# Performance work log

Measured on AMD Instinct MI355X. Metric: run time of the kernel, lower is better.

Reference implementation:

```python
import jax, jax.numpy as jnp
import numpy as np

B, DIM, HEADS, HEAD_DIM = 4, 768, 8, 96
THW = (8, 28, 28)
N_TOK = THW[0] * THW[1] * THW[2] + 1  # +1 cls token = 6273
HIDDEN = 4 * DIM
STRIDE = (1, 2, 2)
SCALE = HEAD_DIM ** -0.5


def layernorm(x, w, b, eps=1e-5):
    mu = x.mean(-1, keepdims=True)
    var = ((x - mu) ** 2).mean(-1, keepdims=True)
    return (x - mu) / jnp.sqrt(var + eps) * w + b


def conv_pool(x, w):
    # depthwise 3D conv: x [BN, C, T, H, W], w [C, 1, 3, 3, 3], stride (1,2,2), pad 1
    return jax.lax.conv_general_dilated(
        x, w, window_strides=STRIDE, padding=[(1, 1), (1, 1), (1, 1)],
        dimension_numbers=('NCDHW', 'OIDHW', 'NCDHW'),
        feature_group_count=x.shape[1])


def attn_pool(x, conv_w, norm_w, norm_b):
    # x: [B, h, N, d]; pool spatial tokens (excluding cls), then LayerNorm(head_dim)
    cls, xs = x[:, :, :1], x[:, :, 1:]
    b, h, _, d = xs.shape
    t, hh, ww = THW
    xs = xs.reshape(b * h, t, hh, ww, d).transpose(0, 4, 1, 2, 3)  # [bh, d, t, h, w]
    xs = conv_pool(xs, conv_w)
    l_pooled = xs.shape[2] * xs.shape[3] * xs.shape[4]
    xs = xs.reshape(b, h, d, l_pooled).transpose(0, 1, 3, 2)  # [B, h, L, d]
    xs = jnp.concatenate([cls, xs], axis=2)
    return layernorm(xs, norm_w, norm_b)


def max_pool_skip(x):
    # residual-path MaxPool3d: kernel (1,3,3), stride (1,2,2), pad (0,1,1); cls excluded
    cls, xs = x[:, :1], x[:, 1:]
    b, _, c = xs.shape
    t, hh, ww = THW
    xs = xs.reshape(b, t, hh, ww, c)
    xs = jax.lax.reduce_window(
        xs, -jnp.inf, jax.lax.max,
        (1, 1, 3, 3, 1), (1, 1, 2, 2, 1),
        [(0, 0), (0, 0), (1, 1), (1, 1), (0, 0)])
    xs = xs.reshape(b, -1, c)
    return jnp.concatenate([cls, xs], axis=1)


def setup_inputs() -> dict:
    key = jax.random.key(0)
    ks = jax.random.split(key, 16)
    s = 0.02
    inp = {
        'x': jax.random.normal(ks[0], (B, N_TOK, DIM), jnp.float32),
        'n1_w': jnp.ones((DIM,), jnp.float32), 'n1_b': jnp.zeros((DIM,), jnp.float32),
        'wq': jax.random.normal(ks[1], (DIM, DIM), jnp.float32) * s,
        'bq': jnp.zeros((DIM,), jnp.float32),
        'wk': jax.random.normal(ks[2], (DIM, DIM), jnp.float32) * s,
        'bk': jnp.zeros((DIM,), jnp.float32),
        'wv': jax.random.normal(ks[3], (DIM, DIM), jnp.float32) * s,
        'bv': jnp.zeros((DIM,), jnp.float32),
        'pq_w': jax.random.normal(ks[4], (HEAD_DIM, 1, 3, 3, 3), jnp.float32) * s,
        'pk_w': jax.random.normal(ks[5], (HEAD_DIM, 1, 3, 3, 3), jnp.float32) * s,
        'pv_w': jax.random.normal(ks[6], (HEAD_DIM, 1, 3, 3, 3), jnp.float32) * s,
        'nq_w': jnp.ones((HEAD_DIM,), jnp.float32), 'nq_b': jnp.zeros((HEAD_DIM,), jnp.float32),
        'nk_w': jnp.ones((HEAD_DIM,), jnp.float32), 'nk_b': jnp.zeros((HEAD_DIM,), jnp.float32),
        'nv_w': jnp.ones((HEAD_DIM,), jnp.float32), 'nv_b': jnp.zeros((HEAD_DIM,), jnp.float32),
        'proj_w': jax.random.normal(ks[7], (DIM, DIM), jnp.float32) * s,
        'proj_b': jnp.zeros((DIM,), jnp.float32),
        'n2_w': jnp.ones((DIM,), jnp.float32), 'n2_b': jnp.zeros((DIM,), jnp.float32),
        'fc1_w': jax.random.normal(ks[8], (HIDDEN, DIM), jnp.float32) * s,
        'fc1_b': jnp.zeros((HIDDEN,), jnp.float32),
        'fc2_w': jax.random.normal(ks[9], (DIM, HIDDEN), jnp.float32) * s,
        'fc2_b': jnp.zeros((DIM,), jnp.float32),
    }
    return inp


def reference(x, n1_w, n1_b, wq, bq, wk, bk, wv, bv, pq_w, pk_w, pv_w,
              nq_w, nq_b, nk_w, nk_b, nv_w, nv_b, proj_w, proj_b,
              n2_w, n2_b, fc1_w, fc1_b, fc2_w, fc2_b):
    b, n, _ = x.shape
    xn = layernorm(x, n1_w, n1_b)
    # q/k/v projections -> [B, h, N, d]
    q = (xn @ wq.T + bq).reshape(b, n, HEADS, HEAD_DIM).transpose(0, 2, 1, 3)
    k = (xn @ wk.T + bk).reshape(b, n, HEADS, HEAD_DIM).transpose(0, 2, 1, 3)
    v = (xn @ wv.T + bv).reshape(b, n, HEADS, HEAD_DIM).transpose(0, 2, 1, 3)
    q = attn_pool(q, pq_w, nq_w, nq_b)
    k = attn_pool(k, pk_w, nk_w, nk_b)
    v = attn_pool(v, pv_w, nv_w, nv_b)
    attn = jax.nn.softmax(jnp.einsum('bhqd,bhkd->bhqk', q, k) * SCALE, axis=-1)
    o = jnp.einsum('bhqk,bhkd->bhqd', attn, v)
    nq = o.shape[2]
    o = o.transpose(0, 2, 1, 3).reshape(b, nq, DIM)
    o = o @ proj_w.T + proj_b
    # residual with pooled skip
    x2 = max_pool_skip(x) + o
    xn2 = layernorm(x2, n2_w, n2_b)
    m = jax.nn.gelu(xn2 @ fc1_w.T + fc1_b, approximate=False) @ fc2_w.T + fc2_b
    return x2 + m
```

## Files before the change

kernel.cpp:

```cpp
#include <hip/hip_runtime.h>
#include <math.h>

#define B_ 4
#define NTOK 6273
#define DIMD 768
#define HEADS 8
#define HD 96
#define NPOOL 1569
#define NPAD 1600
#define HID 3072
#define MROWS (B_*NTOK)
#define M2 (B_*NPOOL)
#define SCALE_ 0.10206207261596575f

typedef float f32x4 __attribute__((ext_vector_type(4)));
typedef short s16x8 __attribute__((ext_vector_type(8)));
typedef short s16x4 __attribute__((ext_vector_type(4)));
typedef unsigned u32x3 __attribute__((ext_vector_type(3)));

__device__ __forceinline__ short f2bf(float f){
  unsigned u = __builtin_bit_cast(unsigned, f);
  u = (u + 0x7fffu + ((u >> 16) & 1u)) >> 16;
  return (short)u;
}
__device__ __forceinline__ float bf2f(short s){
  unsigned u = ((unsigned)(unsigned short)s) << 16;
  return __builtin_bit_cast(float, u);
}
__device__ __forceinline__ float bfsel(unsigned u, int hi){
  unsigned r = hi ? (u & 0xffff0000u) : (u << 16);
  return __builtin_bit_cast(float, r);
}
__device__ __forceinline__ unsigned pack2(float lo, float hi){
  return (unsigned)(unsigned short)f2bf(lo) | ((unsigned)(unsigned short)f2bf(hi) << 16);
}

__device__ __forceinline__ void gld16(const void* g, void* l){
  __builtin_amdgcn_global_load_lds((const __attribute__((address_space(1))) unsigned*)g,
                                   (__attribute__((address_space(3))) unsigned*)l, 16, 0, 0);
}

#if defined(__has_builtin)
#if __has_builtin(__builtin_amdgcn_mfma_f32_16x16x16bf16_1k)
#define MFMA16K(a,b,c) __builtin_amdgcn_mfma_f32_16x16x16bf16_1k(a,b,c,0,0,0)
#endif
#endif
#ifndef MFMA16K
__device__ __forceinline__ f32x4 mfma16k_asm(s16x4 a, s16x4 b, f32x4 c){
  asm volatile("v_mfma_f32_16x16x16_bf16 %0, %1, %2, %0\n\ts_nop 7\n\ts_nop 7"
               : "+v"(c) : "v"(a), "v"(b));
  return c;
}
#define MFMA16K(a,b,c) mfma16k_asm(a,b,c)
#endif

template<int NT>
__device__ __forceinline__ float block_sum(float v, float* red){
  int t = threadIdx.x;
  red[t] = v; __syncthreads();
  #pragma unroll
  for (int s = NT/2; s > 0; s >>= 1){
    if (t < s) red[t] += red[t+s];
    __syncthreads();
  }
  float r = red[0];
  __syncthreads();
  return r;
}

__device__ __forceinline__ unsigned xcd_serial(unsigned bid, unsigned nwg){
  unsigned q = nwg >> 3, r8 = nwg & 7;
  unsigned xcd = bid & 7, idx = bid >> 3;
  return (xcd < r8 ? xcd*(q+1) : r8*(q+1) + (xcd-r8)*q) + idx;
}

template<int STR, int STC>
__device__ __forceinline__ void tile_decode(unsigned serial, int& rowT, int& colT){
  const int nStC = (int)gridDim.x / STC;
  int st = (int)serial / (STR*STC);
  int t  = (int)serial - st*(STR*STC);
  int stR = st / nStC, stC = st - stR*nStC;
  int c = t / STR, r = t - c*STR;
  rowT = stR*STR + r;
  colT = stC*STC + c;
}

__global__ void castw(const float* s0,const float* s1,const float* s2,const float* s3,
                      const float* s4,const float* s5,
                      short* d0,short* d1,short* d2,short* d3,short* d4,short* d5){
  const float* s; short* d; int n;
  switch(blockIdx.y){
    case 0: s=s0; d=d0; n=589824; break;
    case 1: s=s1; d=d1; n=589824; break;
    case 2: s=s2; d=d2; n=589824; break;
    case 3: s=s3; d=d3; n=589824; break;
    case 4: s=s4; d=d4; n=2359296; break;
    default: s=s5; d=d5; n=2359296; break;
  }
  for (int i = blockIdx.x*blockDim.x + threadIdx.x; i < n; i += gridDim.x*blockDim.x)
    d[i] = f2bf(s[i]);
}

__global__ __launch_bounds__(256) void packb(const float* b0, const float* b1, const float* b2, float* o){
  int i = blockIdx.x*256 + threadIdx.x;
  if (i < 768) o[i] = b0[i];
  else if (i < 1536) o[i] = b1[i-768];
  else if (i < 2304) o[i] = b2[i-1536];
}

__global__ __launch_bounds__(256) void ln768(const float* __restrict__ x, const float* __restrict__ w,
                      const float* __restrict__ b, short* __restrict__ out){
  int row = blockIdx.x*4 + (threadIdx.x >> 6);
  int lane = threadIdx.x & 63;
  const float* xr = x + (size_t)row*DIMD + lane*12;
  f32x4 v0 = *(const f32x4*)(xr);
  f32x4 v1 = *(const f32x4*)(xr + 4);
  f32x4 v2 = *(const f32x4*)(xr + 8);
  float v[12] = { v0[0],v0[1],v0[2],v0[3], v1[0],v1[1],v1[2],v1[3], v2[0],v2[1],v2[2],v2[3] };
  float s = 0.f;
  #pragma unroll
  for (int j=0;j<12;j++) s += v[j];
  #pragma unroll
  for (int m=1; m<64; m<<=1) s += __shfl_xor(s, m);
  float mu = s * (1.f/768.f);
  float sq = 0.f;
  #pragma unroll
  for (int j=0;j<12;j++){ float d = v[j]-mu; sq += d*d; }
  #pragma unroll
  for (int m=1; m<64; m<<=1) sq += __shfl_xor(sq, m);
  float rstd = rsqrtf(sq*(1.f/768.f) + 1e-5f);
  int c0 = lane*12;
  float o[12];
  #pragma unroll
  for (int j=0;j<12;j++) o[j] = (v[j]-mu)*rstd*w[c0+j] + b[c0+j];
  unsigned* po = (unsigned*)(out + (size_t)row*DIMD + c0);
  #pragma unroll
  for (int k=0;k<6;k++) po[k] = pack2(o[2*k], o[2*k+1]);
}

__global__ __launch_bounds__(512) void gemm8(const short* __restrict__ A, const short* __restrict__ Bw,
                        const float* __restrict__ bias, short* __restrict__ Cb,
                        int M, int N, int K){
  __shared__ short lds[4][16384];
  int tid = threadIdx.x;
  int w = tid >> 6, lane = tid & 63;
  int l15 = lane & 15, g = (lane >> 4) & 3;
  int wr = w >> 2, wc = w & 3;

  unsigned nwg = gridDim.x * gridDim.y;
  unsigned bid = blockIdx.y * gridDim.x + blockIdx.x;
  unsigned serial = bid;
  if (nwg >= 512) serial = xcd_serial(bid, nwg);
  int rowBase = (int)(serial / gridDim.x) * 256;
  int colBase = (int)(serial % gridDim.x) * 256;

  const short* pa[2]; const short* pb[2];
  #pragma unroll
  for (int j=0;j<2;j++){
    int mr = rowBase + (w + j*8)*16 + l15; if (mr >= M) mr = M-1;
    int nr = colBase + (w + j*8)*16 + l15;
    pa[j] = A  + (size_t)mr*K + g*8;
    pb[j] = Bw + (size_t)nr*K + g*8;
  }
  int sd = tid*8;

  auto stage = [&](int slot, int p){
    int koff = p*32;
    short* base = &lds[slot][0];
    #pragma unroll
    for (int j=0;j<2;j++){
      gld16(pa[j] + koff, base + sd + j*4096);
      gld16(pb[j] + koff, base + 8192 + sd + j*4096);
    }
  };

  f32x4 acc[8][4] = {};
  int np = K >> 5;
  stage(0, 0);
  if (np > 1) stage(1, 1);
  if (np > 2) stage(2, 2);
  for (int p = 0; p < np; p++){
    if (p <= np-3)
      asm volatile("s_waitcnt vmcnt(8)" ::: "memory");
    else if (p == np-2)
      asm volatile("s_waitcnt vmcnt(4)" ::: "memory");
    else
      asm volatile("s_waitcnt vmcnt(0)" ::: "memory");
    __builtin_amdgcn_s_barrier();
    if (p + 3 < np) stage((p+3)&3, p+3);
    const short* lA = &lds[p&3][0];
    const short* lB = lA + 8192;
    s16x8 bfr[4];
    #pragma unroll
    for (int nf=0; nf<4; nf++)
      bfr[nf] = *(const s16x8*)(lB + (wc*4+nf)*512 + lane*8);
    __builtin_amdgcn_s_setprio(1);
    #pragma unroll
    for (int mf=0; mf<8; mf++){
      s16x8 af = *(const s16x8*)(lA + (wr*8+mf)*512 + lane*8);
      #pragma unroll
      for (int nf=0; nf<4; nf++)
        acc[mf][nf] = __builtin_amdgcn_mfma_f32_16x16x32_bf16(af, bfr[nf], acc[mf][nf], 0,0,0);
    }
    __builtin_amdgcn_s_setprio(0);
  }

  __syncthreads();
  short* ldsC = &lds[0][0];
  #pragma unroll
  for (int mf=0; mf<8; mf++){
    int rowL0 = wr*128 + mf*16 + g*4;
    #pragma unroll
    for (int nf=0; nf<4; nf++){
      int colL = wc*64 + nf*16 + l15;
      float bv = bias[colBase + colL];
      int ch = colL >> 3, in8 = colL & 7;
      #pragma unroll
      for (int r=0;r<4;r++){
        int rL = rowL0 + r;
        int chs = ch ^ ((rL >> 2) & 7);
        ldsC[rL*256 + chs*8 + in8] = f2bf(acc[mf][nf][r] + bv);
      }
    }
  }
  __syncthreads();
  int ch2 = tid & 31, rg = tid >> 5;
  #pragma unroll
  for (int i=0;i<16;i++){
    int rowL = rg + i*16;
    int chs = ch2 ^ ((rowL >> 2) & 7);
    s16x8 v = *(const s16x8*)(ldsC + rowL*256 + chs*8);
    int rr = rowBase + rowL;
    if (rr < M) *(s16x8*)(Cb + (size_t)rr*N + colBase + ch2*8) = v;
  }
}

template<int GELU, int OUTBF16, int RESID, int STR, int STC>
__global__ __launch_bounds__(256) void gemm_bt(const short* __restrict__ A, const short* __restrict__ Bw,
                        const float* __restrict__ bias, const float* __restrict__ resid,
                        float* __restrict__ Cf, short* __restrict__ Cb,
                        int M, int N, int K){
  __shared__ short lds[3][8192];
  int tid = threadIdx.x;
  int lane = tid & 63, wv = tid >> 6;
  int wr = wv >> 1, wc = wv & 1;
  int l15 = lane & 15, g = lane >> 4;

  unsigned nwg = gridDim.x * gridDim.y;
  unsigned bid = blockIdx.y * gridDim.x + blockIdx.x;
  unsigned serial = xcd_serial(bid, nwg);
  int rowT, colT;
  tile_decode<STR,STC>(serial, rowT, colT);
  int rowBase = rowT * 128;
  int colBase = colT * 128;

  f32x4 acc[4][4] = {};
  int srow = (tid & 15) | ((tid >> 6) << 4);
  int scol = ((tid >> 4) & 3) * 8;
  int ldsoff = tid * 8;

  int ar0 = rowBase + srow;      if (ar0 >= M) ar0 = M-1;
  int ar1 = rowBase + srow + 64; if (ar1 >= M) ar1 = M-1;
  int br0 = colBase + srow;
  const short* pa0 = A  + (size_t)ar0*K + scol;
  const short* pa1 = A  + (size_t)ar1*K + scol;
  const short* pb0 = Bw + (size_t)br0*K + scol;
  const short* pb1 = Bw + (size_t)(br0+64)*K + scol;

  auto stage = [&](int s, int kt){
    gld16(pa0 + kt, &lds[s][ldsoff]);
    gld16(pa1 + kt, &lds[s][ldsoff + 2048]);
    gld16(pb0 + kt, &lds[s][4096 + ldsoff]);
    gld16(pb1 + kt, &lds[s][4096 + ldsoff + 2048]);
  };

  int nk = K >> 5;
  stage(0, 0);
  if (nk > 1) stage(1, 32);
  for (int kt = 0; kt < nk; kt++){
    int cur = kt % 3;
    if (kt + 2 < nk){
      stage((kt+2)%3, (kt+2)*32);
      asm volatile("s_waitcnt vmcnt(8)" ::: "memory");
    } else if (kt + 1 < nk){
      asm volatile("s_waitcnt vmcnt(4)" ::: "memory");
    } else {
      asm volatile("s_waitcnt vmcnt(0)" ::: "memory");
    }
    __builtin_amdgcn_s_barrier();
    const short* la = lds[cur];
    const short* lb = lds[cur] + 4096;
    s16x8 af[4], bfr[4];
    #pragma unroll
    for (int m=0;m<4;m++) af[m]  = *(const s16x8*)(la + (wr*4 + m)*512 + g*128 + l15*8);
    #pragma unroll
    for (int n=0;n<4;n++) bfr[n] = *(const s16x8*)(lb + (wc*4 + n)*512 + g*128 + l15*8);
    #pragma unroll
    for (int m=0;m<4;m++)
      #pragma unroll
      for (int n=0;n<4;n++)
        acc[m][n] = __builtin_amdgcn_mfma_f32_16x16x32_bf16(af[m], bfr[n], acc[m][n], 0,0,0);
    __builtin_amdgcn_s_barrier();
  }

  if (OUTBF16){
    short* ldsC = &lds[0][0];
    #pragma unroll
    for (int n=0;n<4;n++){
      int colL = wc*64 + n*16 + l15;
      float bv = bias[colBase + colL];
      #pragma unroll
      for (int m=0;m<4;m++){
        #pragma unroll
        for (int r=0;r<4;r++){
          int rowL = wr*64 + m*16 + g*4 + r;
          float v = acc[m][n][r] + bv;
          if (GELU) v = 0.5f*v*(1.f + erff(v*0.70710678118654752f));
          int ch = colL >> 3, in8 = colL & 7;
          int chs = ch ^ (((rowL >> 2) & 3) << 2);
          ldsC[rowL*128 + chs*8 + in8] = f2bf(v);
        }
      }
    }
    __syncthreads();
    int ch = tid & 15, rg = tid >> 4;
    #pragma unroll
    for (int i=0;i<8;i++){
      int rowL = rg + i*16;
      int chs = ch ^ (((rowL >> 2) & 3) << 2);
      s16x8 v = *(const s16x8*)(ldsC + rowL*128 + chs*8);
      int rr = rowBase + rowL;
      if (rr < M) *(s16x8*)(Cb + (size_t)rr*N + colBase + ch*8) = v;
    }
  } else {
    #pragma unroll
    for (int m=0;m<4;m++){
      int row = rowBase + wr*64 + m*16 + g*4;
      #pragma unroll
      for (int n=0;n<4;n++){
        int col = colBase + wc*64 + n*16 + l15;
        float bv = bias[col];
        #pragma unroll
        for (int r=0;r<4;r++){
          int rr = row + r;
          if (rr < M){
            float v = acc[m][n][r] + bv;
            if (GELU) v = 0.5f*v*(1.f + erff(v*0.70710678118654752f));
            if (RESID) v += resid[(size_t)rr*N + col];
            Cf[(size_t)rr*N + col] = v;
          }
        }
      }
    }
  }
}

__global__ __launch_bounds__(256, 2) void pool_conv3(
    const short* __restrict__ raw,
    const float* __restrict__ cwq, const float* __restrict__ cwk, const float* __restrict__ cwv,
    const float* __restrict__ nqw, const float* __restrict__ nqb,
    const float* __restrict__ nkw, const float* __restrict__ nkb,
    const float* __restrict__ nvw, const float* __restrict__ nvb,
    short* __restrict__ qo, short* __restrict__ ko, short* __restrict__ vo){
  unsigned nwg = gridDim.x * gridDim.y * gridDim.z;
  unsigned lin = (blockIdx.z*gridDim.y + blockIdx.y)*gridDim.x + blockIdx.x;
  unsigned serial = xcd_serial(lin, nwg);
  int ho = (int)(serial % 14);
  unsigned rest = serial / 14;
  int bh = (int)(rest & 31);
  int z  = (int)(rest >> 5);
  int t = threadIdx.x;
  int g = t >> 4;
  if (g >= 14) return;
  int s = t & 15, d = s*6;
  const float* cw = (z==0) ? cwq : (z==1) ? cwk : cwv;
  const float* nw = (z==0) ? nqw : (z==1) ? nkw : nvw;
  const float* nb = (z==0) ? nqb : (z==1) ? nkb : nvb;
  const short* base = raw + (size_t)(bh>>3)*NTOK*2304 + z*768 + (bh&7)*96 + d;
  float acc[8][6] = {};
  #pragma unroll
  for (int dh=0; dh<3; dh++){
    int ih = 2*ho - 1 + dh;
    if (ih < 0 || ih >= 28) continue;
    #pragma unroll
    for (int dw=0; dw<3; dw++){
      int iw = 2*g - 1 + dw;
      if (iw < 0 || iw >= 28) continue;
      float w[3][6];
      #pragma unroll
      for (int dt=0; dt<3; dt++)
        #pragma unroll
        for (int j=0;j<6;j++)
          w[dt][j] = cw[(d+j)*27 + dt*9 + dh*3 + dw];
      #pragma unroll
      for (int it=0; it<8; it++){
        u32x3 u = *(const u32x3*)(base + (size_t)(1 + (it*28+ih)*28 + iw)*2304);
        float in[6] = { bfsel(u[0],0), bfsel(u[0],1), bfsel(u[1],0),
                        bfsel(u[1],1), bfsel(u[2],0), bfsel(u[2],1) };
        #pragma unroll
        for (int dt=0; dt<3; dt++){
          int to = it + 1 - dt;
          if (to < 0 || to > 7) continue;
          #pragma unroll
          for (int j=0;j<6;j++) acc[to][j] = fmaf(in[j], w[dt][j], acc[to][j]);
        }
      }
    }
  }
  float nwv[6], nbv[6];
  #pragma unroll
  for (int j=0;j<6;j++){ nwv[j] = nw[d+j]; nbv[j] = nb[d+j]; }
  #pragma unroll
  for (int to=0; to<8; to++){
    float sm = acc[to][0]+acc[to][1]+acc[to][2]+acc[to][3]+acc[to][4]+acc[to][5];
    #pragma unroll
    for (int m=1; m<16; m<<=1) sm += __shfl_xor(sm, m);
    float mu = sm*(1.f/96.f);
    float vr = 0.f;
    #pragma unroll
    for (int j=0;j<6;j++){ float dd = acc[to][j]-mu; vr += dd*dd; }
    #pragma unroll
    for (int m=1; m<16; m<<=1) vr += __shfl_xor(vr, m);
    float rstd = rsqrtf(vr*(1.f/96.f) + 1e-5f);
    int tok = 1 + to*196 + ho*14 + g;
    if (z == 0){
      short o[6];
      #pragma unroll
      for (int j=0;j<6;j++) o[j] = f2bf((acc[to][j]-mu)*rstd*nwv[j] + nbv[j]);
      unsigned* q32 = (unsigned*)(qo + ((size_t)bh*NPAD + tok)*96 + d);
      #pragma unroll
      for (int w2=0; w2<3; w2++)
        q32[w2] = (unsigned)(unsigned short)o[2*w2] | ((unsigned)(unsigned short)o[2*w2+1] << 16);
    } else if (z == 1){
      size_t kb = (size_t)bh*NPAD*96 + (size_t)(tok>>4)*1536 + (tok&15)*8;
      #pragma unroll
      for (int j=0;j<6;j++){
        int dj = d + j;
        ko[kb + (dj>>5)*512 + ((dj>>3)&3)*128 + (dj&7)] = f2bf((acc[to][j]-mu)*rstd*nwv[j] + nbv[j]);
      }
    } else {
      size_t vb = (size_t)bh*NPAD*96 + (size_t)(tok>>6)*6144 + ((tok>>4)&3)*256 + ((tok>>2)&3)*64 + (tok&3);
      #pragma unroll
      for (int j=0;j<6;j++){
        int dj = d + j;
        vo[vb + (dj>>4)*1024 + (dj&15)*4] = f2bf((acc[to][j]-mu)*rstd*nwv[j] + nbv[j]);
      }
    }
  }
}

__global__ __launch_bounds__(128) void cls3(
    const short* __restrict__ raw,
    const float* __restrict__ nqw, const float* __restrict__ nqb,
    const float* __restrict__ nkw, const float* __restrict__ nkb,
    const float* __restrict__ nvw, const float* __restrict__ nvb,
    short* __restrict__ qo, short* __restrict__ ko, short* __restrict__ vo){
  int b = blockIdx.x, t = threadIdx.x;
  int h = t >> 4, s = t & 15, d = s*6;
  int bh = b*8 + h;
  const float* nws[3] = { nqw, nkw, nvw };
  const float* nbs[3] = { nqb, nkb, nvb };
  #pragma unroll
  for (int ten=0; ten<3; ten++){
    const short* row = raw + (size_t)b*NTOK*2304 + ten*768 + h*96 + d;
    u32x3 u = *(const u32x3*)(row);
    float a[6] = { bfsel(u[0],0), bfsel(u[0],1), bfsel(u[1],0), bfsel(u[1],1), bfsel(u[2],0), bfsel(u[2],1) };
    float sm = a[0]+a[1]+a[2]+a[3]+a[4]+a[5];
    #pragma unroll
    for (int m=1; m<16; m<<=1) sm += __shfl_xor(sm, m);
    float mu = sm*(1.f/96.f);
    float vr2 = 0.f;
    #pragma unroll
    for (int j=0;j<6;j++){ float dd = a[j]-mu; vr2 += dd*dd; }
    #pragma unroll
    for (int m=1; m<16; m<<=1) vr2 += __shfl_xor(vr2, m);
    float rstd = rsqrtf(vr2*(1.f/96.f) + 1e-5f);
    #pragma unroll
    for (int j=0;j<6;j++){
      int dj = d + j;
      short o = f2bf((a[j]-mu)*rstd*nws[ten][dj] + nbs[ten][dj]);
      if (ten == 0)      qo[((size_t)bh*NPAD)*96 + dj] = o;
      else if (ten == 1) ko[(size_t)bh*NPAD*96 + (dj>>5)*512 + ((dj>>3)&3)*128 + (dj&7)] = o;
      else               vo[(size_t)bh*NPAD*96 + (dj>>4)*1024 + (dj&15)*4] = o;
    }
  }
}

__global__ __launch_bounds__(96) void padfill(short* __restrict__ qo, short* __restrict__ ko, short* __restrict__ vo){
  int tok = NPOOL + blockIdx.x;
  int bh = blockIdx.y;
  int d = threadIdx.x;
  qo[((size_t)bh*NPAD + tok)*96 + d] = 0;
  size_t kb = (size_t)bh*NPAD*96 + (size_t)(tok>>4)*1536 + (tok&15)*8;
  ko[kb + (d>>5)*512 + ((d>>3)&3)*128 + (d&7)] = 0;
  size_t vb = (size_t)bh*NPAD*96 + (size_t)(tok>>6)*6144 + ((tok>>4)&3)*256 + ((tok>>2)&3)*64 + (tok&3);
  vo[vb + (d>>4)*1024 + (d&15)*4] = 0;
}

__global__ __launch_bounds__(512) void attn_k(const short* __restrict__ qp, const short* __restrict__ kp,
                       const short* __restrict__ vp, short* __restrict__ oattn){
  const float M0 = 6.0f;
  __shared__ short lkv[2][12288];
  unsigned nwg = gridDim.x * gridDim.y;
  unsigned bid0 = blockIdx.y * gridDim.x + blockIdx.x;
  unsigned serial = xcd_serial(bid0, nwg);
  int bh = (int)(serial / 13);
  int qblk = (int)(serial - (unsigned)bh*13);
  int b = bh >> 3, h = bh & 7;
  int tid = threadIdx.x;
  int lane = tid & 63, wv = tid >> 6;
  int l15 = lane & 15, g = lane >> 4;
  int qi = qblk*128 + wv*16 + l15;
  int qi_ld = qi < NPAD ? qi : NPAD-1;
  const short* qbase = qp + (size_t)bh*NPAD*HD;
  const short* kbase = kp + (size_t)bh*NPAD*HD;
  const short* vbase = vp + (size_t)bh*NPAD*HD;
  s16x8 qf[3];
  #pragma unroll
  for (int f=0; f<3; f++)
    qf[f] = *(const s16x8*)(qbase + (size_t)qi_ld*HD + f*32 + g*8);

  auto stage = [&](int bsel, int t){
    #pragma unroll
    for (int i=0;i<3;i++){
      int off = i*4096 + tid*8;
      const short* src = (off < 6144) ? (kbase + t*6144 + off) : (vbase + t*6144 + off - 6144);
      gld16(src, &lkv[bsel][off]);
    }
  };

  f32x4 accO[6] = {};
  float tsum = 0.f;

  stage(0, 0);
  asm volatile("s_waitcnt vmcnt(0)" ::: "memory");
  __builtin_amdgcn_s_barrier();

  for (int kt = 0; kt < 25; kt++){
    int cur = kt & 1;
    if (kt < 24){
      stage(cur^1, kt+1);
      asm volatile("s_waitcnt vmcnt(3)" ::: "memory");
    } else {
      asm volatile("s_waitcnt vmcnt(0)" ::: "memory");
    }
    __builtin_amdgcn_s_barrier();

    const short* lkc = &lkv[cur][0];
    const short* lvc = &lkv[cur][6144];
    f32x4 sacc[4];
    #pragma unroll
    for (int sub=0; sub<4; sub++){
      sacc[sub] = (f32x4){0.f,0.f,0.f,0.f};
      #pragma unroll
      for (int f=0; f<3; f++){
        s16x8 kf = *(const s16x8*)(lkc + sub*1536 + f*512 + lane*8);
        sacc[sub] = __builtin_amdgcn_mfma_f32_16x16x32_bf16(kf, qf[f], sacc[sub], 0,0,0);
      }
    }
    s16x4 pf[4];
    if (kt < 24){
      #pragma unroll
      for (int sub=0; sub<4; sub++){
        #pragma unroll
        for (int r=0; r<4; r++){
          float p = __expf(sacc[sub][r]*SCALE_ - M0);
          tsum += p;
          pf[sub][r] = f2bf(p);
        }
      }
    } else {
      #pragma unroll
      for (int sub=0; sub<4; sub++){
        #pragma unroll
        for (int r=0; r<4; r++){
          int ki = kt*64 + sub*16 + g*4 + r;
          float p = (ki < NPOOL) ? __expf(sacc[sub][r]*SCALE_ - M0) : 0.f;
          tsum += p;
          pf[sub][r] = f2bf(p);
        }
      }
    }
    #pragma unroll
    for (int dt=0; dt<6; dt++){
      #pragma unroll
      for (int sub=0; sub<4; sub++){
        s16x4 vf = *(const s16x4*)(lvc + dt*1024 + sub*256 + lane*4);
        accO[dt] = MFMA16K(vf, pf[sub], accO[dt]);
      }
    }
    __builtin_amdgcn_s_barrier();
  }

  tsum += __shfl_xor(tsum, 16);
  tsum += __shfl_xor(tsum, 32);
  if (qi < NPOOL){
    float inv = 1.f / tsum;
    #pragma unroll
    for (int dt=0; dt<6; dt++){
      #pragma unroll
      for (int r=0; r<4; r++){
        int dd = dt*16 + g*4 + r;
        oattn[((size_t)b*NPOOL + qi)*DIMD + h*96 + dd] = f2bf(accO[dt][r] * inv);
      }
    }
  }
}

__global__ __launch_bounds__(256) void skip_ln2(const float* __restrict__ x, const float* __restrict__ oproj,
                         const float* __restrict__ w, const float* __restrict__ bb,
                         float* __restrict__ x2, short* __restrict__ xn2){
  unsigned nwg = gridDim.x * gridDim.y;
  unsigned bid = blockIdx.y * gridDim.x + blockIdx.x;
  unsigned serial = xcd_serial(bid, nwg);
  int b = (int)(serial / NPOOL);
  int tok = (int)(serial - (unsigned)b*NPOOL);
  int t = threadIdx.x;
  __shared__ float red[256];
  float v[3];
  int ot = tok - 1;
  int to = ot/196, rem = ot%196, ho = rem/14, wo = rem%14;
  #pragma unroll
  for (int i=0;i<3;i++){
    int c = t + i*256;
    float mv;
    if (tok == 0){
      mv = x[(size_t)b*NTOK*DIMD + c];
    } else {
      mv = -INFINITY;
      #pragma unroll
      for (int dh=0; dh<3; dh++){
        int ih = 2*ho - 1 + dh; if (ih < 0 || ih >= 28) continue;
        #pragma unroll
        for (int dw=0; dw<3; dw++){
          int iw = 2*wo - 1 + dw; if (iw < 0 || iw >= 28) continue;
          int n = 1 + (to*28 + ih)*28 + iw;
          mv = fmaxf(mv, x[((size_t)b*NTOK + n)*DIMD + c]);
        }
      }
    }
    float val = mv + oproj[((size_t)b*NPOOL + tok)*DIMD + c];
    x2[((size_t)b*NPOOL + tok)*DIMD + c] = val;
    v[i] = val;
  }
  float s = v[0]+v[1]+v[2];
  s = block_sum<256>(s, red);
  float mu = s * (1.f/768.f);
  float sq = 0.f;
  #pragma unroll
  for (int i=0;i<3;i++){ float d = v[i]-mu; sq += d*d; }
  sq = block_sum<256>(sq, red);
  float rstd = rsqrtf(sq*(1.f/768.f) + 1e-5f);
  #pragma unroll
  for (int i=0;i<3;i++){
    int c = t + i*256;
    xn2[((size_t)b*NPOOL + tok)*DIMD + c] = f2bf((v[i]-mu)*rstd*w[c] + bb[c]);
  }
}

extern "C" void kernel_launch(void* const* d_in, const int* in_sizes, int n_in,
                              void* d_out, int out_size, void* d_ws, size_t ws_size,
                              hipStream_t stream){
  (void)in_sizes; (void)n_in; (void)out_size; (void)ws_size;
  const float* x      = (const float*)d_in[0];
  const float* n1_w   = (const float*)d_in[1];
  const float* n1_b   = (const float*)d_in[2];
  const float* wq     = (const float*)d_in[3];
  const float* bq     = (const float*)d_in[4];
  const float* wk     = (const float*)d_in[5];
  const float* bk     = (const float*)d_in[6];
  const float* wv     = (const float*)d_in[7];
  const float* bv     = (const float*)d_in[8];
  const float* pq_w   = (const float*)d_in[9];
  const float* pk_w   = (const float*)d_in[10];
  const float* pv_w   = (const float*)d_in[11];
  const float* nq_w   = (const float*)d_in[12];
  const float* nq_b   = (const float*)d_in[13];
  const float* nk_w   = (const float*)d_in[14];
  const float* nk_b   = (const float*)d_in[15];
  const float* nv_w   = (const float*)d_in[16];
  const float* nv_b   = (const float*)d_in[17];
  const float* proj_w = (const float*)d_in[18];
  const float* proj_b = (const float*)d_in[19];
  const float* n2_w   = (const float*)d_in[20];
  const float* n2_b   = (const float*)d_in[21];
  const float* fc1_w  = (const float*)d_in[22];
  const float* fc1_b  = (const float*)d_in[23];
  const float* fc2_w  = (const float*)d_in[24];
  const float* fc2_b  = (const float*)d_in[25];
  float* out = (float*)d_out;

  char* ws = (char*)d_ws;
  size_t off = 0;
  auto take = [&](size_t bytes)->char*{
    char* p = ws + off; off = (off + bytes + 255) & ~(size_t)255; return p;
  };
  short* xn  = (short*)take(38541312);
  short* wqb = (short*)take(1179648);
  short* wkb = (short*)take(1179648);
  short* wvb = (short*)take(1179648);
  short* wpb = (short*)take(1179648);
  short* w1b = (short*)take(4718592);
  short* w2b = (short*)take(4718592);
  float* bcat= (float*)take(9216);
  char*  big = take(115623936);
  short* qkv  = (short*)(big);
  short* oattn= (short*)(big);
  float* oproj= (float*)(big + 9639936);
  float* x2   = (float*)(big + 28919808);
  short* xn2  = (short*)(big + 48199680);
  short* h1   = (short*)(big + 57839616);
  short* qp   = (short*)take(9830400);
  short* kp   = (short*)take(9830400);
  short* vT   = (short*)take(9830400);

  castw<<<dim3(2304,6), 256, 0, stream>>>(wq,wk,wv,proj_w,fc1_w,fc2_w, wqb,wkb,wvb,wpb,w1b,w2b);
  packb<<<9, 256, 0, stream>>>(bq, bk, bv, bcat);
  ln768<<<6273, 256, 0, stream>>>(x, n1_w, n1_b, xn);

  gemm8<<<dim3(9,99), 512, 0, stream>>>(xn, wqb, bcat, qkv, MROWS, 2304, 768);

  pool_conv3<<<dim3(32,14,3), 256, 0, stream>>>(qkv, pq_w, pk_w, pv_w,
                                                nq_w, nq_b, nk_w, nk_b, nv_w, nv_b, qp, kp, vT);
  cls3<<<dim3(B_), 128, 0, stream>>>(qkv, nq_w, nq_b, nk_w, nk_b, nv_w, nv_b, qp, kp, vT);
  padfill<<<dim3(31,32), 96, 0, stream>>>(qp, kp, vT);

  attn_k<<<dim3(13,32), 512, 0, stream>>>(qp, kp, vT, oattn);

  gemm_bt<0,0,0,10,6><<<dim3(6,50), 256, 0, stream>>>(oattn, wpb, proj_b, nullptr, oproj, nullptr, M2, 768, 768);

  skip_ln2<<<dim3(NPOOL,B_), 256, 0, stream>>>(x, oproj, n2_w, n2_b, x2, xn2);

  gemm_bt<1,1,0,10,8><<<dim3(24,50), 256, 0, stream>>>(xn2, w1b, fc1_b, nullptr, nullptr, h1, M2, HID, 768);
  gemm_bt<0,0,1,2,3><<<dim3(6,50), 256, 0, stream>>>(h1, w2b, fc2_b, x2, out, nullptr, M2, 768, HID);
}
```

Baseline: 614.6 us.

## Restructure gemm8 main loop into an 8-phase ping-pong schedule with 64-wide K tiles

```diff
diff --git a/kernel.cpp b/kernel.cpp
--- a/kernel.cpp
+++ b/kernel.cpp
@@ -138,14 +138,45 @@
   for (int k=0;k<6;k++) po[k] = pack2(o[2*k], o[2*k+1]);
 }
 
+template<int MH>
+__device__ __forceinline__ void ld_af(s16x8 (&af)[4][2], const short* lA, int lane){
+  #pragma unroll
+  for (int m2=0;m2<4;m2++)
+    #pragma unroll
+    for (int ks=0;ks<2;ks++)
+      af[m2][ks] = *(const s16x8*)(lA + ((MH*4+m2)*2+ks)*512 + lane*8);
+}
+template<int NH>
+__device__ __forceinline__ void ld_bf(s16x8 (&bf)[2][2], const short* lB, int wc1, int lane){
+  #pragma unroll
+  for (int n2=0;n2<2;n2++)
+    #pragma unroll
+    for (int ks=0;ks<2;ks++)
+      bf[n2][ks] = *(const s16x8*)(lB + ((wc1*4+NH*2+n2)*2+ks)*512 + lane*8);
+}
+template<int MH,int NH>
+__device__ __forceinline__ void mm_phase(f32x4 (&acc)[2][2][4][2], const s16x8 (&af)[4][2], const s16x8 (&bf)[2][2]){
+  asm volatile("s_waitcnt lgkmcnt(0)" ::: "memory");
+  __builtin_amdgcn_sched_barrier(0);
+  __builtin_amdgcn_s_setprio(1);
+  #pragma unroll
+  for (int m2=0;m2<4;m2++)
+    #pragma unroll
+    for (int n2=0;n2<2;n2++)
+      #pragma unroll
+      for (int ks=0;ks<2;ks++)
+        acc[MH][NH][m2][n2] = __builtin_amdgcn_mfma_f32_16x16x32_bf16(af[m2][ks], bf[n2][ks], acc[MH][NH][m2][n2], 0,0,0);
+  __builtin_amdgcn_s_setprio(0);
+}
+
 __global__ __launch_bounds__(512) void gemm8(const short* __restrict__ A, const short* __restrict__ Bw,
                         const float* __restrict__ bias, short* __restrict__ Cb,
                         int M, int N, int K){
-  __shared__ short lds[4][16384];
+  __shared__ short lds[65536];
   int tid = threadIdx.x;
   int w = tid >> 6, lane = tid & 63;
   int l15 = lane & 15, g = (lane >> 4) & 3;
-  int wr = w >> 2, wc = w & 3;
+  int wr = w >> 2, wc = w & 3, wc1 = wc & 1;
 
   unsigned nwg = gridDim.x * gridDim.y;
   unsigned bid = blockIdx.y * gridDim.x + blockIdx.x;
@@ -154,72 +185,112 @@
   int rowBase = (int)(serial / gridDim.x) * 256;
   int colBase = (int)(serial % gridDim.x) * 256;
 
-  const short* pa[2]; const short* pb[2];
-  #pragma unroll
-  for (int j=0;j<2;j++){
-    int mr = rowBase + (w + j*8)*16 + l15; if (mr >= M) mr = M-1;
-    int nr = colBase + (w + j*8)*16 + l15;
-    pa[j] = A  + (size_t)mr*K + g*8;
-    pb[j] = Bw + (size_t)nr*K + g*8;
-  }
-  int sd = tid*8;
-
-  auto stage = [&](int slot, int p){
-    int koff = p*32;
-    short* base = &lds[slot][0];
-    #pragma unroll
-    for (int j=0;j<2;j++){
-      gld16(pa[j] + koff, base + sd + j*4096);
-      gld16(pb[j] + koff, base + 8192 + sd + j*4096);
-    }
+  const short* pa[2][2]; const short* pb[2][2];
+  #pragma unroll
+  for (int h=0;h<2;h++){
+    #pragma unroll
+    for (int c=0;c<2;c++){
+      int fw = c*8 + w;
+      int fb = fw >> 1, ks = fw & 1;
+      int mr = rowBase + h*128 + fb*16 + l15; if (mr >= M) mr = M-1;
+      int nr = colBase + h*128 + fb*16 + l15;
+      pa[h][c] = A  + (size_t)mr*K + ks*32 + g*8;
+      pb[h][c] = Bw + (size_t)nr*K + ks*32 + g*8;
+    }
+  }
+
+  auto stageA = [&](int buf, int h, int kt){
+    short* dst = &lds[buf*32768 + h*8192 + tid*8];
+    gld16(pa[h][0] + kt*64, dst);
+    gld16(pa[h][1] + kt*64, dst + 4096);
   };
-
-  f32x4 acc[8][4] = {};
-  int np = K >> 5;
-  stage(0, 0);
-  if (np > 1) stage(1, 1);
-  if (np > 2) stage(2, 2);
-  for (int p = 0; p < np; p++){
-    if (p <= np-3)
-      asm volatile("s_waitcnt vmcnt(8)" ::: "memory");
-    else if (p == np-2)
-      asm volatile("s_waitcnt vmcnt(4)" ::: "memory");
-    else
-      asm volatile("s_waitcnt vmcnt(0)" ::: "memory");
-    __builtin_amdgcn_s_barrier();
-    if (p + 3 < np) stage((p+3)&3, p+3);
-    const short* lA = &lds[p&3][0];
-    const short* lB = lA + 8192;
-    s16x8 bfr[4];
-    #pragma unroll
-    for (int nf=0; nf<4; nf++)
-      bfr[nf] = *(const s16x8*)(lB + (wc*4+nf)*512 + lane*8);
-    __builtin_amdgcn_s_setprio(1);
-    #pragma unroll
-    for (int mf=0; mf<8; mf++){
-      s16x8 af = *(const s16x8*)(lA + (wr*8+mf)*512 + lane*8);
-      #pragma unroll
-      for (int nf=0; nf<4; nf++)
-        acc[mf][nf] = __builtin_amdgcn_mfma_f32_16x16x32_bf16(af, bfr[nf], acc[mf][nf], 0,0,0);
-    }
-    __builtin_amdgcn_s_setprio(0);
+  auto stageB = [&](int buf, int h, int kt){
+    short* dst = &lds[buf*32768 + (2+h)*8192 + tid*8];
+    gld16(pb[h][0] + kt*64, dst);
+    gld16(pb[h][1] + kt*64, dst + 4096);
+  };
+
+  f32x4 acc[2][2][4][2] = {};
+  s16x8 af[4][2], bf[2][2];
+
+  const short* lAx = &lds[wr*8192];
+  const short* lBx = &lds[16384 + (wc>>1)*8192];
+  const short* lAy = lAx + 32768;
+  const short* lBy = lBx + 32768;
+
+  stageA(0,0,0); stageA(0,1,0); stageB(0,0,0); stageB(0,1,0);
+  stageA(1,0,1);
+  asm volatile("s_waitcnt vmcnt(2)" ::: "memory");
+  __builtin_amdgcn_s_barrier();
+
+  for (int i = 0; i < 6; i++){
+    int kx = 2*i;
+    const bool full = (i < 5);
+
+    ld_af<0>(af, lAx, lane); ld_bf<0>(bf, lBx, wc1, lane);
+    stageA(1,1,kx+1);
+    __builtin_amdgcn_s_barrier();
+    mm_phase<0,0>(acc, af, bf);
+    __builtin_amdgcn_s_barrier();
+    ld_bf<1>(bf, lBx, wc1, lane);
+    stageB(1,0,kx+1);
+    __builtin_amdgcn_s_barrier();
+    mm_phase<0,1>(acc, af, bf);
+    __builtin_amdgcn_s_barrier();
+    ld_af<1>(af, lAx, lane);
+    stageB(1,1,kx+1);
+    __builtin_amdgcn_s_barrier();
+    mm_phase<1,1>(acc, af, bf);
+    __builtin_amdgcn_s_barrier();
+    ld_bf<0>(bf, lBx, wc1, lane);
+    if (full){ stageA(0,0,kx+2); asm volatile("s_waitcnt vmcnt(2)" ::: "memory"); }
+    else     { asm volatile("s_waitcnt vmcnt(0)" ::: "memory"); }
+    __builtin_amdgcn_s_barrier();
+    mm_phase<1,0>(acc, af, bf);
+    __builtin_amdgcn_s_barrier();
+    ld_af<0>(af, lAy, lane); ld_bf<0>(bf, lBy, wc1, lane);
+    if (full) stageA(0,1,kx+2);
+    __builtin_amdgcn_s_barrier();
+    mm_phase<0,0>(acc, af, bf);
+    __builtin_amdgcn_s_barrier();
+    ld_bf<1>(bf, lBy, wc1, lane);
+    if (full) stageB(0,0,kx+2);
+    __builtin_amdgcn_s_barrier();
+    mm_phase<0,1>(acc, af, bf);
+    __builtin_amdgcn_s_barrier();
+    ld_af<1>(af, lAy, lane);
+    if (full) stageB(0,1,kx+2);
+    __builtin_amdgcn_s_barrier();
+    mm_phase<1,1>(acc, af, bf);
+    __builtin_amdgcn_s_barrier();
+    ld_bf<0>(bf, lBy, wc1, lane);
+    if (full){ stageA(1,0,kx+3); asm volatile("s_waitcnt vmcnt(2)" ::: "memory"); }
+    __builtin_amdgcn_s_barrier();
+    mm_phase<1,0>(acc, af, bf);
+    __builtin_amdgcn_s_barrier();
   }
 
   __syncthreads();
-  short* ldsC = &lds[0][0];
-  #pragma unroll
-  for (int mf=0; mf<8; mf++){
-    int rowL0 = wr*128 + mf*16 + g*4;
-    #pragma unroll
-    for (int nf=0; nf<4; nf++){
-      int colL = wc*64 + nf*16 + l15;
-      float bv = bias[colBase + colL];
-      int ch = colL >> 3, in8 = colL & 7;
-      #pragma unroll
-      for (int r=0;r<4;r++){
-        int rL = rowL0 + r;
-        int chs = ch ^ ((rL >> 2) & 7);
-        ldsC[rL*256 + chs*8 + in8] = f2bf(acc[mf][nf][r] + bv);
+  short* ldsC = &lds[0];
+  #pragma unroll
+  for (int mh=0; mh<2; mh++){
+    #pragma unroll
+    for (int m2=0; m2<4; m2++){
+      int rowL0 = wr*128 + mh*64 + m2*16 + g*4;
+      #pragma unroll
+      for (int nh=0; nh<2; nh++){
+        #pragma unroll
+        for (int n2=0; n2<2; n2++){
+          int colL = wc*64 + nh*32 + n2*16 + l15;
+          float bv = bias[colBase + colL];
+          int ch = colL >> 3, in8 = colL & 7;
+          #pragma unroll
+          for (int r=0;r<4;r++){
+            int rL = rowL0 + r;
+            int chs = ch ^ ((rL >> 2) & 7);
+            ldsC[rL*256 + chs*8 + in8] = f2bf(acc[mh][nh][m2][n2][r] + bv);
+          }
+        }
       }
     }
   }
```

Result: slower. 631.0 us (+2.7%).

## Add 64x128-tile GEMM kernel for proj and fc2 to raise workgroup count

Applied to the files above, without the earlier changes.

```diff
diff --git a/kernel.cpp b/kernel.cpp
--- a/kernel.cpp
+++ b/kernel.cpp
@@ -349,6 +349,86 @@
             if (RESID) v += resid[(size_t)rr*N + col];
             Cf[(size_t)rr*N + col] = v;
           }
+        }
+      }
+    }
+  }
+}
+
+template<int RESID>
+__global__ __launch_bounds__(256) void gemm_n64(const short* __restrict__ A, const short* __restrict__ Bw,
+                        const float* __restrict__ bias, const float* __restrict__ resid,
+                        float* __restrict__ Cf, int M, int N, int K){
+  __shared__ short lds[3][6144];
+  int tid = threadIdx.x;
+  int lane = tid & 63, wc = tid >> 6;
+  int l15 = lane & 15, g = lane >> 4;
+
+  unsigned nwg = gridDim.x * gridDim.y;
+  unsigned bid = blockIdx.y * gridDim.x + blockIdx.x;
+  unsigned serial = xcd_serial(bid, nwg);
+  int rowBase = (int)(serial / gridDim.x) * 64;
+  int colBase = (int)(serial % gridDim.x) * 128;
+
+  f32x4 acc[4][2] = {};
+  int srow = (tid & 15) | ((tid >> 6) << 4);
+  int scol = ((tid >> 4) & 3) * 8;
+  int ldsoff = tid * 8;
+
+  int ar = rowBase + srow; if (ar >= M) ar = M-1;
+  int br = colBase + srow;
+  const short* pa  = A  + (size_t)ar*K + scol;
+  const short* pb0 = Bw + (size_t)br*K + scol;
+  const short* pb1 = Bw + (size_t)(br+64)*K + scol;
+
+  auto stage = [&](int s, int kt){
+    gld16(pa  + kt, &lds[s][ldsoff]);
+    gld16(pb0 + kt, &lds[s][2048 + ldsoff]);
+    gld16(pb1 + kt, &lds[s][4096 + ldsoff]);
+  };
+
+  int nk = K >> 5;
+  stage(0, 0);
+  if (nk > 1) stage(1, 32);
+  for (int kt = 0; kt < nk; kt++){
+    int cur = kt % 3;
+    if (kt + 2 < nk){
+      stage((kt+2)%3, (kt+2)*32);
+      asm volatile("s_waitcnt vmcnt(6)" ::: "memory");
+    } else if (kt + 1 < nk){
+      asm volatile("s_waitcnt vmcnt(3)" ::: "memory");
+    } else {
+      asm volatile("s_waitcnt vmcnt(0)" ::: "memory");
+    }
+    __builtin_amdgcn_s_barrier();
+    const short* la = lds[cur];
+    const short* lb = lds[cur] + 2048;
+    s16x8 af[4], bfr[2];
+    #pragma unroll
+    for (int m=0;m<4;m++) af[m]  = *(const s16x8*)(la + m*512 + g*128 + l15*8);
+    #pragma unroll
+    for (int n=0;n<2;n++) bfr[n] = *(const s16x8*)(lb + (wc*2 + n)*512 + g*128 + l15*8);
+    #pragma unroll
+    for (int m=0;m<4;m++)
+      #pragma unroll
+      for (int n=0;n<2;n++)
+        acc[m][n] = __builtin_amdgcn_mfma_f32_16x16x32_bf16(af[m], bfr[n], acc[m][n], 0,0,0);
+    __builtin_amdgcn_s_barrier();
+  }
+  #pragma unroll
+  for (int m=0;m<4;m++){
+    int row = rowBase + m*16 + g*4;
+    #pragma unroll
+    for (int n=0;n<2;n++){
+      int col = colBase + wc*32 + n*16 + l15;
+      float bv = bias[col];
+      #pragma unroll
+      for (int r=0;r<4;r++){
+        int rr = row + r;
+        if (rr < M){
+          float v = acc[m][n][r] + bv;
+          if (RESID) v += resid[(size_t)rr*N + col];
+          Cf[(size_t)rr*N + col] = v;
         }
       }
     }
@@ -727,10 +807,10 @@
 
   attn_k<<<dim3(13,32), 512, 0, stream>>>(qp, kp, vT, oattn);
 
-  gemm_bt<0,0,0,10,6><<<dim3(6,50), 256, 0, stream>>>(oattn, wpb, proj_b, nullptr, oproj, nullptr, M2, 768, 768);
+  gemm_n64<0><<<dim3(6,99), 256, 0, stream>>>(oattn, wpb, proj_b, nullptr, oproj, M2, 768, 768);
 
   skip_ln2<<<dim3(NPOOL,B_), 256, 0, stream>>>(x, oproj, n2_w, n2_b, x2, xn2);
 
   gemm_bt<1,1,0,10,8><<<dim3(24,50), 256, 0, stream>>>(xn2, w1b, fc1_b, nullptr, nullptr, h1, M2, HID, 768);
-  gemm_bt<0,0,1,2,3><<<dim3(6,50), 256, 0, stream>>>(h1, w2b, fc2_b, x2, out, nullptr, M2, 768, HID);
-}
+  gemm_n64<1><<<dim3(6,99), 256, 0, stream>>>(h1, w2b, fc2_b, x2, out, M2, 768, 3072);
+}
```

After: 599.6 us. 2.4% less time.
